# Optimization experiments

Measured on AMD Instinct MI355X. Metric: run time of the kernel, lower is better.

The kernel has to match this reference:

```python
import jax, jax.numpy as jnp
import numpy as np

H = W = 128; WS = 8; SHIFT = 4; HEADS = 4; T = 2; EPS = 1e-5
N = WS * WS  # tokens per window per frame


def _rel_pos_index(ws):
    ch, cw = np.meshgrid(np.arange(ws), np.arange(ws), indexing='ij')
    coords = np.stack([ch, cw]).reshape(2, -1)  # (2, N)
    rel = coords[:, :, None] - coords[:, None, :]  # (2, N, N)
    rel = rel.transpose(1, 2, 0)
    rel[:, :, 0] += ws - 1
    rel[:, :, 1] += ws - 1
    rel[:, :, 0] *= 2 * ws - 1
    return rel.sum(-1)  # (N, N) int


def _attn_mask(h, w, ws, shift):
    img = np.zeros((h, w))
    cnt = 0
    for hs in (slice(0, -ws), slice(-ws, -shift), slice(-shift, None)):
        for wsl in (slice(0, -ws), slice(-ws, -shift), slice(-shift, None)):
            img[hs, wsl] = cnt
            cnt += 1
    mw = img.reshape(h // ws, ws, w // ws, ws).transpose(0, 2, 1, 3).reshape(-1, ws * ws)
    diff = mw[:, None, :] - mw[:, :, None]
    return np.where(diff != 0, -100.0, 0.0).astype(np.float32)  # (nW, N, N)


REL_IDX = jnp.asarray(_rel_pos_index(WS))
ATTN_MASK = jnp.asarray(_attn_mask(H, W, WS, SHIFT))


def _ln(x, g, b):
    mu = x.mean(-1, keepdims=True)
    var = ((x - mu) ** 2).mean(-1, keepdims=True)
    return (x - mu) * jax.lax.rsqrt(var + EPS) * g + b


def setup_inputs() -> dict:
    key = jax.random.key(0)
    ks = jax.random.split(key, 8)
    B, C = 4, 128
    hid = 4 * C
    s = 0.02
    return {
        'x_v': jax.random.normal(ks[0], (B, T, H * W, C), jnp.float32),
        'qkv_w': jax.random.normal(ks[1], (3 * C, C), jnp.float32) * s,
        'qkv_b': jnp.zeros((3 * C,), jnp.float32),
        'proj_w': jax.random.normal(ks[2], (C, C), jnp.float32) * s,
        'proj_b': jnp.zeros((C,), jnp.float32),
        'rpb_table': jax.random.normal(ks[3], ((2 * WS - 1) ** 2, HEADS), jnp.float32) * s,
        'norm1_w': jnp.ones((C,), jnp.float32),
        'norm1_b': jnp.zeros((C,), jnp.float32),
        'norm2_w': jnp.ones((C,), jnp.float32),
        'norm2_b': jnp.zeros((C,), jnp.float32),
        'fc1_w': jax.random.normal(ks[4], (hid, C), jnp.float32) * s,
        'fc1_b': jnp.zeros((hid,), jnp.float32),
        'fc2_w': jax.random.normal(ks[5], (C, hid), jnp.float32) * s,
        'fc2_b': jnp.zeros((C,), jnp.float32),
    }


def reference(x_v, qkv_w, qkv_b, proj_w, proj_b, rpb_table,
              norm1_w, norm1_b, norm2_w, norm2_b,
              fc1_w, fc1_b, fc2_w, fc2_b):
    B, Tt, L, C = x_v.shape
    hd = C // HEADS
    nWh, nWw = H // WS, W // WS
    nW = nWh * nWw
    TN = T * N

    shortcut = x_v.reshape(B * T, L, C)
    x = x_v.reshape(B * T, H, W, C)
    x = jnp.roll(x, (-SHIFT, -SHIFT), axis=(1, 2))
    # window partition: (B*T, nWh, ws, nWw, ws, C) -> (B*nW, T, N, C)
    x = x.reshape(B * T, nWh, WS, nWw, WS, C).transpose(0, 1, 3, 2, 4, 5)
    x = x.reshape(B, T, nW, N, C).transpose(0, 2, 1, 3, 4).reshape(B * nW, T, N, C)

    # --- window attention over T*N tokens ---
    B_ = B * nW
    xf = x.reshape(B_, TN, C)
    qkv = xf @ qkv_w.T + qkv_b  # (B_, TN, 3C)
    qkv = qkv.reshape(B_, TN, 3, HEADS, hd).transpose(2, 0, 3, 1, 4)
    q, k, v = qkv[0], qkv[1], qkv[2]  # (B_, heads, TN, hd)
    q = q * (hd ** -0.5)
    attn = jnp.einsum('bhqd,bhkd->bhqk', q, k)  # (B_, heads, TN, TN)

    rpb = rpb_table[REL_IDX.reshape(-1)].reshape(N, N, HEADS).transpose(2, 0, 1)
    rpb = jnp.tile(rpb, (1, T, T))  # (heads, TN, TN)
    attn = attn + rpb[None]

    mask = jnp.tile(ATTN_MASK, (1, T, T))  # (nW, TN, TN)
    attn = attn.reshape(B, nW, HEADS, TN, TN) + mask[None, :, None]
    attn = jax.nn.softmax(attn.reshape(B_, HEADS, TN, TN), axis=-1)

    out = jnp.einsum('bhqk,bhkd->bhqd', attn, v)  # (B_, heads, TN, hd)
    out = out.transpose(0, 2, 1, 3).reshape(B_, T, N, C)
    out = out.reshape(B_ * T * N, C) @ proj_w.T + proj_b
    out = out.reshape(B_, T, N, C)

    # window reverse: (B*nW, T, N, C) -> (B, T, H, W, C)
    x = out.reshape(B, nWh, nWw, T, WS, WS, C).transpose(0, 3, 1, 4, 2, 5, 6)
    x = x.reshape(B * T, H, W, C)
    x = jnp.roll(x, (SHIFT, SHIFT), axis=(1, 2)).reshape(B * T, L, C)

    x = shortcut + x
    h = _ln(x, norm2_w, norm2_b)
    h = jax.nn.gelu(h @ fc1_w.T + fc1_b, approximate=False) @ fc2_w.T + fc2_b
    x = _ln(x + h, norm1_w, norm1_b)
    return x.reshape(B, T, L, C)
```

## Files before the change

### kernel.cpp

```cpp
#include <hip/hip_runtime.h>

typedef unsigned short us;
typedef short s16x8 __attribute__((ext_vector_type(8)));
typedef float f32x4 __attribute__((ext_vector_type(4)));

__device__ __forceinline__ us f2bf(float f) {
  union { float f; unsigned u; } v; v.f = f;
  unsigned u = v.u;
  u += 0x7fffu + ((u >> 16) & 1u);
  return (us)(u >> 16);
}
__device__ __forceinline__ float bf2f(us u) {
  union { unsigned u; float f; } v; v.u = ((unsigned)u) << 16; return v.f;
}
__device__ __forceinline__ s16x8 ld8(const us* p) { return *(const s16x8*)p; }

#define MFMA(a, b, c) __builtin_amdgcn_mfma_f32_16x16x32_bf16(a, b, c, 0, 0, 0)

__device__ __forceinline__ void lds_fence() {
  asm volatile("s_waitcnt lgkmcnt(0)" ::: "memory");
}

__device__ __forceinline__ float qsum(float v) {
  v += __shfl_xor(v, 1, 64); v += __shfl_xor(v, 2, 64);
  v += __shfl_xor(v, 4, 64); v += __shfl_xor(v, 8, 64);
  return v;
}

__device__ __forceinline__ float gelu_fast(float x) {
  float x2 = x * x;
  float nz = x * (-1.5957691216f - 0.0713548163f * x2);
  float e = __expf(nz);
  return x * __builtin_amdgcn_rcpf(1.f + e);
}

__global__ void prep_kernel(const float* __restrict__ qkv_w, const float* __restrict__ proj_w,
                            const float* __restrict__ fc1_w, const float* __restrict__ fc2_w,
                            const float* __restrict__ rpb_table,
                            us* __restrict__ qkvw, us* __restrict__ projw,
                            us* __restrict__ fc1w, us* __restrict__ fc2w,
                            us* __restrict__ rpbm) {
  int id = blockIdx.x * 256 + threadIdx.x;
  if (id < 49152) {
    int n = id % 384, k = id / 384;
    float v = qkv_w[n * 128 + k];
    if (n < 128) v *= 0.17677669529663687f;
    qkvw[(((k >> 3) * 384 + n) << 3) + (k & 7)] = f2bf(v);
    return;
  }
  id -= 49152;
  if (id < 16384) { int n = id % 128, k = id / 128;
    projw[(((k >> 3) * 128 + n) << 3) + (k & 7)] = f2bf(proj_w[n * 128 + k]); return; }
  id -= 16384;
  if (id < 65536) {
    int n = id % 512, k = id / 512;
    int cc = n >> 6, ni = (n >> 4) & 3, c16v = n & 15;
    int ks = k >> 5, qd = (k >> 3) & 3, j = k & 7;
    fc1w[cc * 8192 + (ks * 4 + ni) * 512 + (qd * 16 + c16v) * 8 + j] = f2bf(fc1_w[n * 128 + k]);
    return; }
  id -= 65536;
  if (id < 65536) {
    int n = id % 128, k = id / 128;
    int cc = k >> 6, ks2 = (k >> 5) & 1, qd = (k >> 3) & 3, j = k & 7;
    int ni = n >> 4, c16v = n & 15;
    fc2w[cc * 8192 + (ks2 * 8 + ni) * 512 + (qd * 16 + c16v) * 8 + j] = f2bf(fc2_w[n * 512 + k]);
    return; }
  id -= 65536;
  {
    int h = id >> 14, cls = (id >> 12) & 3, e = id & 4095;
    int n1 = e >> 6, n2 = e & 63;
    int r1 = n1 >> 3, c1 = n1 & 7, r2 = n2 >> 3, c2 = n2 & 7;
    int cH = cls >> 1, cW = cls & 1;
    int cq = (cH ? (r1 < 4 ? 1 : 2) : 0) * 3 + (cW ? (c1 < 4 ? 1 : 2) : 0);
    int ck = (cH ? (r2 < 4 ? 1 : 2) : 0) * 3 + (cW ? (c2 < 4 ? 1 : 2) : 0);
    int ridx = (r1 - r2 + 7) * 15 + (c1 - c2 + 7);
    float v = rpb_table[ridx * 4 + h] + (cq != ck ? -100.f : 0.f);
    rpbm[id] = f2bf(v);
  }
}

__global__ __launch_bounds__(512, 2) void qkv_attn_kernel(
    const float* __restrict__ x_v, const us* __restrict__ qkvw,
    const float* __restrict__ qkv_b, const us* __restrict__ rpbm,
    us* __restrict__ attn_out) {
  __shared__ __align__(16) unsigned char smem[139264];
  us* A   = (us*)smem;
  us* Qs  = (us*)smem;
  us* Ks  = (us*)(smem + 34816);
  us* Vts = (us*)(smem + 69632);

  int w = blockIdx.x;
  int b = w >> 8, wi = w & 255, wh = wi >> 4, ww = wi & 15;
  int tid = threadIdx.x;

  {
    int token = tid >> 2, q = tid & 3;
    int t = token >> 6, n = token & 63, r = n >> 3, c = n & 7;
    int hs = (wh * 8 + r + 4) & 127, wsc = (ww * 8 + c + 4) & 127;
    const float* src = x_v + (size_t)((b * 2 + t) * 16384 + hs * 128 + wsc) * 128 + q * 32;
    us* dst = A + token * 136 + q * 32;
#pragma unroll
    for (int i = 0; i < 4; ++i) {
      float4 f0 = ((const float4*)src)[2 * i];
      float4 f1 = ((const float4*)src)[2 * i + 1];
      s16x8 v;
      v[0] = (short)f2bf(f0.x); v[1] = (short)f2bf(f0.y);
      v[2] = (short)f2bf(f0.z); v[3] = (short)f2bf(f0.w);
      v[4] = (short)f2bf(f1.x); v[5] = (short)f2bf(f1.y);
      v[6] = (short)f2bf(f1.z); v[7] = (short)f2bf(f1.w);
      *(s16x8*)(dst + i * 8) = v;
    }
  }
  __syncthreads();

  int lane = tid & 63, wv = tid >> 6, quad = lane >> 4, c16 = lane & 15;
  int h = wv >> 1, p = wv & 1;
  int clsid = ((wh == 15) ? 2 : 0) + ((ww == 15) ? 1 : 0);

  int rb = p * 64;
  f32x4 acc[4][6];
#pragma unroll
  for (int mi = 0; mi < 4; ++mi)
#pragma unroll
    for (int ni = 0; ni < 6; ++ni) acc[mi][ni] = (f32x4){0.f, 0.f, 0.f, 0.f};
#pragma unroll
  for (int ks = 0; ks < 4; ++ks) {
    int k0 = ks * 32;
    s16x8 af[4];
#pragma unroll
    for (int mi = 0; mi < 4; ++mi)
      af[mi] = ld8(A + (rb + mi * 16 + c16) * 136 + k0 + quad * 8);
#pragma unroll
    for (int ni = 0; ni < 6; ++ni) {
      int gcol = (ni >> 1) * 128 + h * 32 + (ni & 1) * 16 + c16;
      s16x8 bf = ld8(qkvw + ((((k0 >> 3) + quad) * 384 + gcol) << 3));
#pragma unroll
      for (int mi = 0; mi < 4; ++mi) acc[mi][ni] = MFMA(af[mi], bf, acc[mi][ni]);
    }
  }
  __syncthreads();
#pragma unroll
  for (int ni = 0; ni < 6; ++ni) {
    int part = ni >> 1, colh = (ni & 1) * 16 + c16;
    int col = h * 32 + colh;
    float bias = qkv_b[part * 128 + col];
    if (part == 0) bias *= 0.17677669529663687f;
#pragma unroll
    for (int mi = 0; mi < 4; ++mi)
#pragma unroll
      for (int r = 0; r < 4; ++r) {
        int tok = rb + mi * 16 + quad * 4 + r;
        us v = f2bf(acc[mi][ni][r] + bias);
        if (part == 0) Qs[tok * 136 + col] = v;
        else if (part == 1) Ks[tok * 136 + col] = v;
        else Vts[col * 136 + tok] = v;
      }
  }
  __syncthreads();

  us* Pw = (us*)(smem + 104448 + wv * 4352);
  const us* rsrc = rpbm + ((h * 4 + clsid) << 12);
  int cb = h * 32;

  for (int qq = 0; qq < 4; ++qq) {
    int q0 = (p * 4 + qq) * 16;
    s16x8 aq = ld8(Qs + (q0 + c16) * 136 + cb + quad * 8);
    float rbv[8][4];
#pragma unroll
    for (int nj = 0; nj < 8; ++nj) {
      int nk = (nj * 16 + c16) & 63;
#pragma unroll
      for (int r = 0; r < 4; ++r) {
        int nq = (q0 + quad * 4 + r) & 63;
        rbv[nj][r] = bf2f(rsrc[nq * 64 + nk]);
      }
    }
    f32x4 sacc[8];
#pragma unroll
    for (int nj = 0; nj < 8; ++nj) {
      s16x8 bk = ld8(Ks + (nj * 16 + c16) * 136 + cb + quad * 8);
      f32x4 z = (f32x4){0.f, 0.f, 0.f, 0.f};
      sacc[nj] = MFMA(aq, bk, z);
    }
    float sm[4] = {0.f, 0.f, 0.f, 0.f};
#pragma unroll
    for (int nj = 0; nj < 8; ++nj)
#pragma unroll
      for (int r = 0; r < 4; ++r) {
        float pp = __expf(sacc[nj][r] + rbv[nj][r]);
        sacc[nj][r] = pp;
        sm[r] += pp;
      }
    float inv[4];
#pragma unroll
    for (int r = 0; r < 4; ++r) inv[r] = 1.f / qsum(sm[r]);
#pragma unroll
    for (int nj = 0; nj < 8; ++nj)
#pragma unroll
      for (int r = 0; r < 4; ++r)
        Pw[(quad * 4 + r) * 136 + nj * 16 + c16] = f2bf(sacc[nj][r] * inv[r]);
    lds_fence();
    f32x4 oacc[2];
    oacc[0] = (f32x4){0.f, 0.f, 0.f, 0.f};
    oacc[1] = (f32x4){0.f, 0.f, 0.f, 0.f};
#pragma unroll
    for (int ks = 0; ks < 4; ++ks) {
      int k0 = ks * 32;
      s16x8 ap = ld8(Pw + c16 * 136 + k0 + quad * 8);
#pragma unroll
      for (int nt = 0; nt < 2; ++nt) {
        s16x8 bv = ld8(Vts + (cb + nt * 16 + c16) * 136 + k0 + quad * 8);
        oacc[nt] = MFMA(ap, bv, oacc[nt]);
      }
    }
#pragma unroll
    for (int nt = 0; nt < 2; ++nt)
#pragma unroll
      for (int r = 0; r < 4; ++r) {
        int tok = q0 + quad * 4 + r;
        attn_out[((size_t)w * 128 + tok) * 128 + cb + nt * 16 + c16] =
            f2bf(oacc[nt][r]);
      }
    lds_fence();
  }
}

__global__ __launch_bounds__(256) void fused_kernel8(
    const us* __restrict__ attn_ws, const us* __restrict__ projw,
    const float* __restrict__ proj_b, const float* __restrict__ x_v,
    const us* __restrict__ fc1w, const us* __restrict__ fc2w,
    const float* __restrict__ fc1_b, const float* __restrict__ fc2_b,
    const float* __restrict__ n2w, const float* __restrict__ n2b,
    const float* __restrict__ n1w, const float* __restrict__ n1b,
    float* __restrict__ out) {
  __shared__ __align__(16) unsigned char smem[50176];
  us* A   = (us*)smem;
  us* Ws1 = (us*)(smem + 17408);
  us* Ws2 = (us*)(smem + 33792);
  int blk = blockIdx.x;
  int w = blk >> 1, hb = (blk & 1) * 64;
  int b = w >> 8, wi = w & 255, wh = wi >> 4, ww = wi & 15;
  int tid = threadIdx.x;
  int lane = tid & 63, wv = tid >> 6, quad = lane >> 4, c16 = lane & 15;
  int r0 = wv * 16;
  us* Hw = (us*)(smem + wv * 2304);

  {
    int lr = r0 + (lane >> 2), q = lane & 3;
    const us* src = attn_ws + ((size_t)w * 128 + hb + lr) * 128 + q * 32;
    us* dst = A + lr * 136 + q * 32;
#pragma unroll
    for (int i = 0; i < 4; ++i) *(s16x8*)(dst + i * 8) = ld8(src + i * 8);
  }

  size_t grow[4];
  float xv[4][8];
#pragma unroll
  for (int r = 0; r < 4; ++r) {
    int tt = hb + r0 + quad * 4 + r;
    int t = tt >> 6, n = tt & 63, rr = n >> 3, cc2 = n & 7;
    int hf = (wh * 8 + rr + 4) & 127, wf = (ww * 8 + cc2 + 4) & 127;
    grow[r] = (size_t)((b * 2 + t) * 16384 + hf * 128 + wf) * 128;
#pragma unroll
    for (int ni = 0; ni < 8; ++ni) xv[r][ni] = x_v[grow[r] + ni * 16 + c16];
  }

  s16x8 st1[4], st2[4];
  {
    const s16x8* s1 = (const s16x8*)fc1w;
    const s16x8* s2 = (const s16x8*)fc2w;
#pragma unroll
    for (int i = 0; i < 4; ++i) { st1[i] = s1[i * 256 + tid]; st2[i] = s2[i * 256 + tid]; }
  }
  lds_fence();

  f32x4 y[8];
#pragma unroll
  for (int ni = 0; ni < 8; ++ni) y[ni] = (f32x4){0.f, 0.f, 0.f, 0.f};
#pragma unroll
  for (int ks = 0; ks < 4; ++ks) {
    int k0 = ks * 32;
    s16x8 af = ld8(A + (r0 + c16) * 136 + k0 + quad * 8);
#pragma unroll
    for (int ni = 0; ni < 8; ++ni) {
      s16x8 bf = ld8(projw + ((((k0 >> 3) + quad) * 128 + ni * 16 + c16) << 3));
      y[ni] = MFMA(af, bf, y[ni]);
    }
  }

  {
    float sum[4] = {0.f, 0.f, 0.f, 0.f}, sq[4] = {0.f, 0.f, 0.f, 0.f};
#pragma unroll
    for (int ni = 0; ni < 8; ++ni) {
      float pb = proj_b[ni * 16 + c16];
#pragma unroll
      for (int r = 0; r < 4; ++r) {
        float v = y[ni][r] + pb + xv[r][ni];
        y[ni][r] = v;
        sum[r] += v; sq[r] += v * v;
      }
    }
#pragma unroll
    for (int r = 0; r < 4; ++r) {
      float s = qsum(sum[r]), q = qsum(sq[r]);
      float mean = s * 0.0078125f;
      float rstd = rsqrtf(q * 0.0078125f - mean * mean + 1e-5f);
      int m = r0 + quad * 4 + r;
#pragma unroll
      for (int ni = 0; ni < 8; ++ni) {
        int col = ni * 16 + c16;
        A[m * 136 + col] = f2bf((y[ni][r] - mean) * rstd * n2w[col] + n2b[col]);
      }
    }
  }
  lds_fence();

  s16x8 afm[4];
#pragma unroll
  for (int ks = 0; ks < 4; ++ks)
    afm[ks] = ld8(A + (r0 + c16) * 136 + ks * 32 + quad * 8);

  f32x4 o[8];
#pragma unroll
  for (int ni = 0; ni < 8; ++ni) o[ni] = (f32x4){0.f, 0.f, 0.f, 0.f};

  for (int cc = 0; cc < 8; ++cc) {
    __syncthreads();
    {
      s16x8* d1 = (s16x8*)Ws1;
      s16x8* d2 = (s16x8*)Ws2;
#pragma unroll
      for (int i = 0; i < 4; ++i) { d1[i * 256 + tid] = st1[i]; d2[i * 256 + tid] = st2[i]; }
    }
    __syncthreads();
    if (cc < 7) {
      const s16x8* s1 = (const s16x8*)fc1w + (cc + 1) * 1024;
      const s16x8* s2 = (const s16x8*)fc2w + (cc + 1) * 1024;
#pragma unroll
      for (int i = 0; i < 4; ++i) { st1[i] = s1[i * 256 + tid]; st2[i] = s2[i * 256 + tid]; }
    }
    f32x4 f[4];
#pragma unroll
    for (int ni = 0; ni < 4; ++ni) f[ni] = (f32x4){0.f, 0.f, 0.f, 0.f};
#pragma unroll
    for (int ks = 0; ks < 4; ++ks)
#pragma unroll
      for (int ni = 0; ni < 4; ++ni) {
        s16x8 bf = ld8(Ws1 + (ks * 4 + ni) * 512 + lane * 8);
        f[ni] = MFMA(afm[ks], bf, f[ni]);
      }
#pragma unroll
    for (int ni = 0; ni < 4; ++ni) {
      float bb = fc1_b[cc * 64 + ni * 16 + c16];
#pragma unroll
      for (int r = 0; r < 4; ++r) {
        float u = f[ni][r] + bb;
        Hw[(quad * 4 + r) * 72 + ni * 16 + c16] = f2bf(gelu_fast(u));
      }
    }
    lds_fence();
#pragma unroll
    for (int ks2 = 0; ks2 < 2; ++ks2) {
      s16x8 ah = ld8(Hw + c16 * 72 + ks2 * 32 + quad * 8);
#pragma unroll
      for (int ni = 0; ni < 8; ++ni) {
        s16x8 bf = ld8(Ws2 + (ks2 * 8 + ni) * 512 + lane * 8);
        o[ni] = MFMA(ah, bf, o[ni]);
      }
    }
    lds_fence();
  }

  {
    float s1v[4] = {0.f, 0.f, 0.f, 0.f}, q1[4] = {0.f, 0.f, 0.f, 0.f};
#pragma unroll
    for (int ni = 0; ni < 8; ++ni) {
      float fb = fc2_b[ni * 16 + c16];
#pragma unroll
      for (int r = 0; r < 4; ++r) {
        float v = o[ni][r] + fb + y[ni][r];
        y[ni][r] = v;
        s1v[r] += v; q1[r] += v * v;
      }
    }
#pragma unroll
    for (int r = 0; r < 4; ++r) {
      float s = qsum(s1v[r]), q = qsum(q1[r]);
      float mean = s * 0.0078125f;
      float rstd = rsqrtf(q * 0.0078125f - mean * mean + 1e-5f);
#pragma unroll
      for (int ni = 0; ni < 8; ++ni) {
        int col = ni * 16 + c16;
        out[grow[r] + col] = (y[ni][r] - mean) * rstd * n1w[col] + n1b[col];
      }
    }
  }
}

extern "C" void kernel_launch(void* const* d_in, const int* in_sizes, int n_in,
                              void* d_out, int out_size, void* d_ws, size_t ws_size,
                              hipStream_t stream) {
  const float* x_v   = (const float*)d_in[0];
  const float* qkv_w = (const float*)d_in[1];
  const float* qkv_b = (const float*)d_in[2];
  const float* proj_w = (const float*)d_in[3];
  const float* proj_b = (const float*)d_in[4];
  const float* rpb_t = (const float*)d_in[5];
  const float* n1w = (const float*)d_in[6];
  const float* n1b = (const float*)d_in[7];
  const float* n2w = (const float*)d_in[8];
  const float* n2b = (const float*)d_in[9];
  const float* fc1_w = (const float*)d_in[10];
  const float* fc1_b = (const float*)d_in[11];
  const float* fc2_w = (const float*)d_in[12];
  const float* fc2_b = (const float*)d_in[13];

  char* ws = (char*)d_ws;
  us* qkvw    = (us*)(ws + 0);
  us* projw   = (us*)(ws + 98304);
  us* fc1w    = (us*)(ws + 131072);
  us* fc2w    = (us*)(ws + 262144);
  us* rpbm    = (us*)(ws + 393216);
  us* attn_ws = (us*)(ws + 524288);

  prep_kernel<<<1024, 256, 0, stream>>>(qkv_w, proj_w, fc1_w, fc2_w, rpb_t,
                                        qkvw, projw, fc1w, fc2w, rpbm);
  qkv_attn_kernel<<<1024, 512, 0, stream>>>(x_v, qkvw, qkv_b, rpbm, attn_ws);
  fused_kernel8<<<2048, 256, 0, stream>>>(attn_ws, projw, proj_b, x_v,
                                          fc1w, fc2w, fc1_b, fc2_b,
                                          n2w, n2b, n1w, n1b, (float*)d_out);
}
```

Before: 278.3 us.

## Double-buffer MLP weight chunks in LDS and pre-swizzle bias/mask for vector loads

The MLP loop now uses 32-wide hidden chunks with two LDS buffers. The next chunk is copied from global memory straight into the alternate buffer, which removes one barrier and the register staging per iteration. The relative-position-bias/mask table is expanded in the prep kernel into a per-lane MFMA fragment layout, so each lane reads its biases with four 16-byte loads instead of 32 scalar gathers. The cost is a table four times larger, twice as many loop iterations, and global loads whose latency now sits on the barrier path.

```diff
diff --git a/kernel.cpp b/kernel.cpp
--- a/kernel.cpp
+++ b/kernel.cpp
@@ -54,28 +54,30 @@
   id -= 16384;
   if (id < 65536) {
     int n = id % 512, k = id / 512;
-    int cc = n >> 6, ni = (n >> 4) & 3, c16v = n & 15;
-    int ks = k >> 5, qd = (k >> 3) & 3, j = k & 7;
-    fc1w[cc * 8192 + (ks * 4 + ni) * 512 + (qd * 16 + c16v) * 8 + j] = f2bf(fc1_w[n * 128 + k]);
+    fc1w[((n >> 5) << 12) + (((k >> 5) * 2 + ((n >> 4) & 1)) << 9)
+         + ((((k >> 3) & 3) * 16 + (n & 15)) << 3) + (k & 7)] = f2bf(fc1_w[n * 128 + k]);
     return; }
   id -= 65536;
   if (id < 65536) {
     int n = id % 128, k = id / 128;
-    int cc = k >> 6, ks2 = (k >> 5) & 1, qd = (k >> 3) & 3, j = k & 7;
-    int ni = n >> 4, c16v = n & 15;
-    fc2w[cc * 8192 + (ks2 * 8 + ni) * 512 + (qd * 16 + c16v) * 8 + j] = f2bf(fc2_w[n * 512 + k]);
+    fc2w[((k >> 5) << 12) + ((n >> 4) << 9)
+         + ((((k >> 3) & 3) * 16 + (n & 15)) << 3) + (k & 7)] = f2bf(fc2_w[n * 512 + k]);
     return; }
   id -= 65536;
   {
-    int h = id >> 14, cls = (id >> 12) & 3, e = id & 4095;
-    int n1 = e >> 6, n2 = e & 63;
-    int r1 = n1 >> 3, c1 = n1 & 7, r2 = n2 >> 3, c2 = n2 & 7;
+    int h = id >> 15, cls = (id >> 13) & 3, qcase = (id >> 11) & 3;
+    int lane = (id >> 5) & 63, v = id & 31;
+    int nj = v >> 2, rr = v & 3;
+    int quad = lane >> 4, c16v = lane & 15;
+    int nq = (qcase * 16 + quad * 4 + rr) & 63;
+    int nk = (nj * 16 + c16v) & 63;
+    int r1 = nq >> 3, c1 = nq & 7, r2 = nk >> 3, c2 = nk & 7;
     int cH = cls >> 1, cW = cls & 1;
     int cq = (cH ? (r1 < 4 ? 1 : 2) : 0) * 3 + (cW ? (c1 < 4 ? 1 : 2) : 0);
     int ck = (cH ? (r2 < 4 ? 1 : 2) : 0) * 3 + (cW ? (c2 < 4 ? 1 : 2) : 0);
     int ridx = (r1 - r2 + 7) * 15 + (c1 - c2 + 7);
-    float v = rpb_table[ridx * 4 + h] + (cq != ck ? -100.f : 0.f);
-    rpbm[id] = f2bf(v);
+    float val = rpb_table[ridx * 4 + h] + (cq != ck ? -100.f : 0.f);
+    rpbm[id] = f2bf(val);
   }
 }
 
@@ -159,22 +161,16 @@
   __syncthreads();
 
   us* Pw = (us*)(smem + 104448 + wv * 4352);
-  const us* rsrc = rpbm + ((h * 4 + clsid) << 12);
+  const us* rsrc = rpbm + (((h * 4 + clsid) * 4) << 11) + lane * 32;
   int cb = h * 32;
 
   for (int qq = 0; qq < 4; ++qq) {
     int q0 = (p * 4 + qq) * 16;
     s16x8 aq = ld8(Qs + (q0 + c16) * 136 + cb + quad * 8);
-    float rbv[8][4];
-#pragma unroll
-    for (int nj = 0; nj < 8; ++nj) {
-      int nk = (nj * 16 + c16) & 63;
-#pragma unroll
-      for (int r = 0; r < 4; ++r) {
-        int nq = (q0 + quad * 4 + r) & 63;
-        rbv[nj][r] = bf2f(rsrc[nq * 64 + nk]);
-      }
-    }
+    const us* rp = rsrc + (((q0 >> 4) & 3) << 11);
+    s16x8 rbv8[4];
+#pragma unroll
+    for (int i = 0; i < 4; ++i) rbv8[i] = ld8(rp + i * 8);
     f32x4 sacc[8];
 #pragma unroll
     for (int nj = 0; nj < 8; ++nj) {
@@ -187,7 +183,7 @@
     for (int nj = 0; nj < 8; ++nj)
 #pragma unroll
       for (int r = 0; r < 4; ++r) {
-        float pp = __expf(sacc[nj][r] + rbv[nj][r]);
+        float pp = __expf(sacc[nj][r] + bf2f((us)rbv8[nj >> 1][((nj & 1) << 2) + r]));
         sacc[nj][r] = pp;
         sm[r] += pp;
       }
@@ -225,7 +221,7 @@
   }
 }
 
-__global__ __launch_bounds__(256) void fused_kernel8(
+__global__ __launch_bounds__(256) void fused_kernel9(
     const us* __restrict__ attn_ws, const us* __restrict__ projw,
     const float* __restrict__ proj_b, const float* __restrict__ x_v,
     const us* __restrict__ fc1w, const us* __restrict__ fc2w,
@@ -234,16 +230,16 @@
     const float* __restrict__ n1w, const float* __restrict__ n1b,
     float* __restrict__ out) {
   __shared__ __align__(16) unsigned char smem[50176];
-  us* A   = (us*)smem;
-  us* Ws1 = (us*)(smem + 17408);
-  us* Ws2 = (us*)(smem + 33792);
+  us* A  = (us*)smem;
+  us* W1 = (us*)(smem + 17408);
+  us* W2 = (us*)(smem + 33792);
   int blk = blockIdx.x;
   int w = blk >> 1, hb = (blk & 1) * 64;
   int b = w >> 8, wi = w & 255, wh = wi >> 4, ww = wi & 15;
   int tid = threadIdx.x;
   int lane = tid & 63, wv = tid >> 6, quad = lane >> 4, c16 = lane & 15;
   int r0 = wv * 16;
-  us* Hw = (us*)(smem + wv * 2304);
+  us* Hw = (us*)(smem + wv * 1280);
 
   {
     int lr = r0 + (lane >> 2), q = lane & 3;
@@ -265,12 +261,14 @@
     for (int ni = 0; ni < 8; ++ni) xv[r][ni] = x_v[grow[r] + ni * 16 + c16];
   }
 
-  s16x8 st1[4], st2[4];
   {
     const s16x8* s1 = (const s16x8*)fc1w;
     const s16x8* s2 = (const s16x8*)fc2w;
-#pragma unroll
-    for (int i = 0; i < 4; ++i) { st1[i] = s1[i * 256 + tid]; st2[i] = s2[i * 256 + tid]; }
+    s16x8* d1 = (s16x8*)W1;
+    s16x8* d2 = (s16x8*)W2;
+#pragma unroll
+    for (int i = 0; i < 2; ++i) { d1[i * 256 + tid] = s1[i * 256 + tid];
+                                  d2[i * 256 + tid] = s2[i * 256 + tid]; }
   }
   lds_fence();
 
@@ -324,49 +322,43 @@
 #pragma unroll
   for (int ni = 0; ni < 8; ++ni) o[ni] = (f32x4){0.f, 0.f, 0.f, 0.f};
 
-  for (int cc = 0; cc < 8; ++cc) {
+  for (int cc = 0; cc < 16; ++cc) {
+    int cur = cc & 1;
     __syncthreads();
-    {
-      s16x8* d1 = (s16x8*)Ws1;
-      s16x8* d2 = (s16x8*)Ws2;
-#pragma unroll
-      for (int i = 0; i < 4; ++i) { d1[i * 256 + tid] = st1[i]; d2[i * 256 + tid] = st2[i]; }
-    }
-    __syncthreads();
-    if (cc < 7) {
-      const s16x8* s1 = (const s16x8*)fc1w + (cc + 1) * 1024;
-      const s16x8* s2 = (const s16x8*)fc2w + (cc + 1) * 1024;
-#pragma unroll
-      for (int i = 0; i < 4; ++i) { st1[i] = s1[i * 256 + tid]; st2[i] = s2[i * 256 + tid]; }
-    }
-    f32x4 f[4];
-#pragma unroll
-    for (int ni = 0; ni < 4; ++ni) f[ni] = (f32x4){0.f, 0.f, 0.f, 0.f};
+    if (cc < 15) {
+      const s16x8* s1 = (const s16x8*)(fc1w + ((cc + 1) << 12));
+      const s16x8* s2 = (const s16x8*)(fc2w + ((cc + 1) << 12));
+      s16x8* d1 = (s16x8*)(W1 + ((cur ^ 1) << 12));
+      s16x8* d2 = (s16x8*)(W2 + ((cur ^ 1) << 12));
+#pragma unroll
+      for (int i = 0; i < 2; ++i) { d1[i * 256 + tid] = s1[i * 256 + tid];
+                                    d2[i * 256 + tid] = s2[i * 256 + tid]; }
+    }
+    const us* w1c = W1 + (cur << 12);
+    const us* w2c = W2 + (cur << 12);
+    f32x4 f[2];
+    f[0] = (f32x4){0.f, 0.f, 0.f, 0.f};
+    f[1] = (f32x4){0.f, 0.f, 0.f, 0.f};
 #pragma unroll
     for (int ks = 0; ks < 4; ++ks)
 #pragma unroll
-      for (int ni = 0; ni < 4; ++ni) {
-        s16x8 bf = ld8(Ws1 + (ks * 4 + ni) * 512 + lane * 8);
+      for (int ni = 0; ni < 2; ++ni) {
+        s16x8 bf = ld8(w1c + ((ks * 2 + ni) << 9) + lane * 8);
         f[ni] = MFMA(afm[ks], bf, f[ni]);
       }
 #pragma unroll
-    for (int ni = 0; ni < 4; ++ni) {
-      float bb = fc1_b[cc * 64 + ni * 16 + c16];
-#pragma unroll
-      for (int r = 0; r < 4; ++r) {
-        float u = f[ni][r] + bb;
-        Hw[(quad * 4 + r) * 72 + ni * 16 + c16] = f2bf(gelu_fast(u));
-      }
+    for (int ni = 0; ni < 2; ++ni) {
+      float bb = fc1_b[cc * 32 + ni * 16 + c16];
+#pragma unroll
+      for (int r = 0; r < 4; ++r)
+        Hw[(quad * 4 + r) * 40 + ni * 16 + c16] = f2bf(gelu_fast(f[ni][r] + bb));
     }
     lds_fence();
-#pragma unroll
-    for (int ks2 = 0; ks2 < 2; ++ks2) {
-      s16x8 ah = ld8(Hw + c16 * 72 + ks2 * 32 + quad * 8);
-#pragma unroll
-      for (int ni = 0; ni < 8; ++ni) {
-        s16x8 bf = ld8(Ws2 + (ks2 * 8 + ni) * 512 + lane * 8);
-        o[ni] = MFMA(ah, bf, o[ni]);
-      }
+    s16x8 ah = ld8(Hw + c16 * 40 + quad * 8);
+#pragma unroll
+    for (int ni = 0; ni < 8; ++ni) {
+      s16x8 bf = ld8(w2c + (ni << 9) + lane * 8);
+      o[ni] = MFMA(ah, bf, o[ni]);
     }
     lds_fence();
   }
@@ -421,12 +413,12 @@
   us* fc1w    = (us*)(ws + 131072);
   us* fc2w    = (us*)(ws + 262144);
   us* rpbm    = (us*)(ws + 393216);
-  us* attn_ws = (us*)(ws + 524288);
-
-  prep_kernel<<<1024, 256, 0, stream>>>(qkv_w, proj_w, fc1_w, fc2_w, rpb_t,
+  us* attn_ws = (us*)(ws + 655360);
+
+  prep_kernel<<<1280, 256, 0, stream>>>(qkv_w, proj_w, fc1_w, fc2_w, rpb_t,
                                         qkvw, projw, fc1w, fc2w, rpbm);
   qkv_attn_kernel<<<1024, 512, 0, stream>>>(x_v, qkvw, qkv_b, rpbm, attn_ws);
-  fused_kernel8<<<2048, 256, 0, stream>>>(attn_ws, projw, proj_b, x_v,
+  fused_kernel9<<<2048, 256, 0, stream>>>(attn_ws, projw, proj_b, x_v,
                                           fc1w, fc2w, fc1_b, fc2_b,
                                           n2w, n2b, n1w, n1b, (float*)d_out);
 }
```

Result: slower. 294.1 us (+5.7%).

## Fuse attention and MLP kernels into one window-level mega kernel

Applied to the files above, without the earlier changes.

Merges the QKV/attention kernel and the proj+MLP kernel into a single kernel per window, keeping the attention output in LDS instead of writing it to a global workspace and reading it back. The rel-pos-bias/mask table is re-laid-out in prep so each lane reads its bias values as contiguous 8-element vectors, and Q fragments are hoisted into registers. The MLP weight chunks are now copied straight from global into LDS each iteration instead of being staged through registers. This removes a launch and a round trip through global memory. In exchange, blocks now hold 512 threads with 136KB of LDS, and the two-blocks-per-CU launch bound is dropped, which may lower occupancy and register headroom.

```diff
diff --git a/kernel.cpp b/kernel.cpp
--- a/kernel.cpp
+++ b/kernel.cpp
@@ -67,27 +67,37 @@
     return; }
   id -= 65536;
   {
-    int h = id >> 14, cls = (id >> 12) & 3, e = id & 4095;
-    int n1 = e >> 6, n2 = e & 63;
-    int r1 = n1 >> 3, c1 = n1 & 7, r2 = n2 >> 3, c2 = n2 & 7;
+    int h = id >> 15, cls = (id >> 13) & 3, qcase = (id >> 11) & 3;
+    int lane = (id >> 5) & 63, v = id & 31;
+    int nj = v >> 2, rr = v & 3;
+    int quad = lane >> 4, c16v = lane & 15;
+    int nq = (qcase * 16 + quad * 4 + rr) & 63;
+    int nk = (nj * 16 + c16v) & 63;
+    int r1 = nq >> 3, c1 = nq & 7, r2 = nk >> 3, c2 = nk & 7;
     int cH = cls >> 1, cW = cls & 1;
     int cq = (cH ? (r1 < 4 ? 1 : 2) : 0) * 3 + (cW ? (c1 < 4 ? 1 : 2) : 0);
     int ck = (cH ? (r2 < 4 ? 1 : 2) : 0) * 3 + (cW ? (c2 < 4 ? 1 : 2) : 0);
     int ridx = (r1 - r2 + 7) * 15 + (c1 - c2 + 7);
-    float v = rpb_table[ridx * 4 + h] + (cq != ck ? -100.f : 0.f);
-    rpbm[id] = f2bf(v);
-  }
-}
-
-__global__ __launch_bounds__(512, 2) void qkv_attn_kernel(
+    float val = rpb_table[ridx * 4 + h] + (cq != ck ? -100.f : 0.f);
+    rpbm[id] = f2bf(val);
+  }
+}
+
+__global__ __launch_bounds__(512) void mega_kernel(
     const float* __restrict__ x_v, const us* __restrict__ qkvw,
     const float* __restrict__ qkv_b, const us* __restrict__ rpbm,
-    us* __restrict__ attn_out) {
+    const us* __restrict__ projw, const float* __restrict__ proj_b,
+    const us* __restrict__ fc1w, const us* __restrict__ fc2w,
+    const float* __restrict__ fc1_b, const float* __restrict__ fc2_b,
+    const float* __restrict__ n2w, const float* __restrict__ n2b,
+    const float* __restrict__ n1w, const float* __restrict__ n1b,
+    float* __restrict__ out) {
   __shared__ __align__(16) unsigned char smem[139264];
   us* A   = (us*)smem;
-  us* Qs  = (us*)smem;
   us* Ks  = (us*)(smem + 34816);
   us* Vts = (us*)(smem + 69632);
+  us* W1  = (us*)(smem + 34816);
+  us* W2  = (us*)(smem + 34816 + 16384);
 
   int w = blockIdx.x;
   int b = w >> 8, wi = w & 255, wh = wi >> 4, ww = wi & 15;
@@ -116,78 +126,79 @@
   int lane = tid & 63, wv = tid >> 6, quad = lane >> 4, c16 = lane & 15;
   int h = wv >> 1, p = wv & 1;
   int clsid = ((wh == 15) ? 2 : 0) + ((ww == 15) ? 1 : 0);
-
-  int rb = p * 64;
-  f32x4 acc[4][6];
-#pragma unroll
-  for (int mi = 0; mi < 4; ++mi)
-#pragma unroll
-    for (int ni = 0; ni < 6; ++ni) acc[mi][ni] = (f32x4){0.f, 0.f, 0.f, 0.f};
-#pragma unroll
-  for (int ks = 0; ks < 4; ++ks) {
-    int k0 = ks * 32;
-    s16x8 af[4];
+  int cb = h * 32;
+
+  {
+    int rb = p * 64;
+    f32x4 acc[4][6];
 #pragma unroll
     for (int mi = 0; mi < 4; ++mi)
-      af[mi] = ld8(A + (rb + mi * 16 + c16) * 136 + k0 + quad * 8);
+#pragma unroll
+      for (int ni = 0; ni < 6; ++ni) acc[mi][ni] = (f32x4){0.f, 0.f, 0.f, 0.f};
+#pragma unroll
+    for (int ks = 0; ks < 4; ++ks) {
+      int k0 = ks * 32;
+      s16x8 af[4];
+#pragma unroll
+      for (int mi = 0; mi < 4; ++mi)
+        af[mi] = ld8(A + (rb + mi * 16 + c16) * 136 + k0 + quad * 8);
+#pragma unroll
+      for (int ni = 0; ni < 6; ++ni) {
+        int gcol = (ni >> 1) * 128 + cb + (ni & 1) * 16 + c16;
+        s16x8 bf = ld8(qkvw + ((((k0 >> 3) + quad) * 384 + gcol) << 3));
+#pragma unroll
+        for (int mi = 0; mi < 4; ++mi) acc[mi][ni] = MFMA(af[mi], bf, acc[mi][ni]);
+      }
+    }
+    __syncthreads();
 #pragma unroll
     for (int ni = 0; ni < 6; ++ni) {
-      int gcol = (ni >> 1) * 128 + h * 32 + (ni & 1) * 16 + c16;
-      s16x8 bf = ld8(qkvw + ((((k0 >> 3) + quad) * 384 + gcol) << 3));
-#pragma unroll
-      for (int mi = 0; mi < 4; ++mi) acc[mi][ni] = MFMA(af[mi], bf, acc[mi][ni]);
+      int part = ni >> 1, colh = (ni & 1) * 16 + c16;
+      int col = cb + colh;
+      float bias = qkv_b[part * 128 + col];
+      if (part == 0) bias *= 0.17677669529663687f;
+#pragma unroll
+      for (int mi = 0; mi < 4; ++mi)
+#pragma unroll
+        for (int r = 0; r < 4; ++r) {
+          int tok = rb + mi * 16 + quad * 4 + r;
+          us v = f2bf(acc[mi][ni][r] + bias);
+          if (part == 0) A[tok * 136 + col] = v;
+          else if (part == 1) Ks[tok * 136 + col] = v;
+          else Vts[col * 136 + tok] = v;
+        }
     }
   }
   __syncthreads();
-#pragma unroll
-  for (int ni = 0; ni < 6; ++ni) {
-    int part = ni >> 1, colh = (ni & 1) * 16 + c16;
-    int col = h * 32 + colh;
-    float bias = qkv_b[part * 128 + col];
-    if (part == 0) bias *= 0.17677669529663687f;
-#pragma unroll
-    for (int mi = 0; mi < 4; ++mi)
-#pragma unroll
-      for (int r = 0; r < 4; ++r) {
-        int tok = rb + mi * 16 + quad * 4 + r;
-        us v = f2bf(acc[mi][ni][r] + bias);
-        if (part == 0) Qs[tok * 136 + col] = v;
-        else if (part == 1) Ks[tok * 136 + col] = v;
-        else Vts[col * 136 + tok] = v;
-      }
-  }
+
+  s16x8 aq[4];
+#pragma unroll
+  for (int qq = 0; qq < 4; ++qq)
+    aq[qq] = ld8(A + ((p * 4 + qq) * 16 + c16) * 136 + cb + quad * 8);
   __syncthreads();
 
   us* Pw = (us*)(smem + 104448 + wv * 4352);
-  const us* rsrc = rpbm + ((h * 4 + clsid) << 12);
-  int cb = h * 32;
+  const us* rsrc = rpbm + (((h * 4 + clsid) * 4) << 11) + lane * 32;
 
   for (int qq = 0; qq < 4; ++qq) {
     int q0 = (p * 4 + qq) * 16;
-    s16x8 aq = ld8(Qs + (q0 + c16) * 136 + cb + quad * 8);
-    float rbv[8][4];
-#pragma unroll
-    for (int nj = 0; nj < 8; ++nj) {
-      int nk = (nj * 16 + c16) & 63;
-#pragma unroll
-      for (int r = 0; r < 4; ++r) {
-        int nq = (q0 + quad * 4 + r) & 63;
-        rbv[nj][r] = bf2f(rsrc[nq * 64 + nk]);
-      }
-    }
+    const us* rp = rsrc + (((q0 >> 4) & 3) << 11);
+    s16x8 rbv8[4];
+#pragma unroll
+    for (int i = 0; i < 4; ++i) rbv8[i] = ld8(rp + i * 8);
     f32x4 sacc[8];
 #pragma unroll
     for (int nj = 0; nj < 8; ++nj) {
       s16x8 bk = ld8(Ks + (nj * 16 + c16) * 136 + cb + quad * 8);
       f32x4 z = (f32x4){0.f, 0.f, 0.f, 0.f};
-      sacc[nj] = MFMA(aq, bk, z);
+      sacc[nj] = MFMA(aq[qq], bk, z);
     }
     float sm[4] = {0.f, 0.f, 0.f, 0.f};
 #pragma unroll
     for (int nj = 0; nj < 8; ++nj)
 #pragma unroll
       for (int r = 0; r < 4; ++r) {
-        float pp = __expf(sacc[nj][r] + rbv[nj][r]);
+        float pp = __expf(sacc[nj][r] + bf2f((us)rbv8[nj >> 1][((nj & 1) << 2) + r]));
         sacc[nj][r] = pp;
         sm[r] += pp;
       }
@@ -218,46 +229,20 @@
 #pragma unroll
       for (int r = 0; r < 4; ++r) {
         int tok = q0 + quad * 4 + r;
-        attn_out[((size_t)w * 128 + tok) * 128 + cb + nt * 16 + c16] =
-            f2bf(oacc[nt][r]);
+        A[tok * 136 + cb + nt * 16 + c16] = f2bf(oacc[nt][r]);
       }
     lds_fence();
   }
-}
-
-__global__ __launch_bounds__(256) void fused_kernel8(
-    const us* __restrict__ attn_ws, const us* __restrict__ projw,
-    const float* __restrict__ proj_b, const float* __restrict__ x_v,
-    const us* __restrict__ fc1w, const us* __restrict__ fc2w,
-    const float* __restrict__ fc1_b, const float* __restrict__ fc2_b,
-    const float* __restrict__ n2w, const float* __restrict__ n2b,
-    const float* __restrict__ n1w, const float* __restrict__ n1b,
-    float* __restrict__ out) {
-  __shared__ __align__(16) unsigned char smem[50176];
-  us* A   = (us*)smem;
-  us* Ws1 = (us*)(smem + 17408);
-  us* Ws2 = (us*)(smem + 33792);
-  int blk = blockIdx.x;
-  int w = blk >> 1, hb = (blk & 1) * 64;
-  int b = w >> 8, wi = w & 255, wh = wi >> 4, ww = wi & 15;
-  int tid = threadIdx.x;
-  int lane = tid & 63, wv = tid >> 6, quad = lane >> 4, c16 = lane & 15;
+  __syncthreads();
+
   int r0 = wv * 16;
-  us* Hw = (us*)(smem + wv * 2304);
-
-  {
-    int lr = r0 + (lane >> 2), q = lane & 3;
-    const us* src = attn_ws + ((size_t)w * 128 + hb + lr) * 128 + q * 32;
-    us* dst = A + lr * 136 + q * 32;
-#pragma unroll
-    for (int i = 0; i < 4; ++i) *(s16x8*)(dst + i * 8) = ld8(src + i * 8);
-  }
+  us* Hw = (us*)(smem + 69632 + wv * 2304);
 
   size_t grow[4];
   float xv[4][8];
 #pragma unroll
   for (int r = 0; r < 4; ++r) {
-    int tt = hb + r0 + quad * 4 + r;
+    int tt = r0 + quad * 4 + r;
     int t = tt >> 6, n = tt & 63, rr = n >> 3, cc2 = n & 7;
     int hf = (wh * 8 + rr + 4) & 127, wf = (ww * 8 + cc2 + 4) & 127;
     grow[r] = (size_t)((b * 2 + t) * 16384 + hf * 128 + wf) * 128;
@@ -265,14 +250,15 @@
     for (int ni = 0; ni < 8; ++ni) xv[r][ni] = x_v[grow[r] + ni * 16 + c16];
   }
 
-  s16x8 st1[4], st2[4];
   {
     const s16x8* s1 = (const s16x8*)fc1w;
     const s16x8* s2 = (const s16x8*)fc2w;
-#pragma unroll
-    for (int i = 0; i < 4; ++i) { st1[i] = s1[i * 256 + tid]; st2[i] = s2[i * 256 + tid]; }
-  }
-  lds_fence();
+    s16x8* d1 = (s16x8*)W1;
+    s16x8* d2 = (s16x8*)W2;
+#pragma unroll
+    for (int i = 0; i < 2; ++i) { d1[i * 512 + tid] = s1[i * 512 + tid];
+                                  d2[i * 512 + tid] = s2[i * 512 + tid]; }
+  }
 
   f32x4 y[8];
 #pragma unroll
@@ -326,19 +312,6 @@
 
   for (int cc = 0; cc < 8; ++cc) {
     __syncthreads();
-    {
-      s16x8* d1 = (s16x8*)Ws1;
-      s16x8* d2 = (s16x8*)Ws2;
-#pragma unroll
-      for (int i = 0; i < 4; ++i) { d1[i * 256 + tid] = st1[i]; d2[i * 256 + tid] = st2[i]; }
-    }
-    __syncthreads();
-    if (cc < 7) {
-      const s16x8* s1 = (const s16x8*)fc1w + (cc + 1) * 1024;
-      const s16x8* s2 = (const s16x8*)fc2w + (cc + 1) * 1024;
-#pragma unroll
-      for (int i = 0; i < 4; ++i) { st1[i] = s1[i * 256 + tid]; st2[i] = s2[i * 256 + tid]; }
-    }
     f32x4 f[4];
 #pragma unroll
     for (int ni = 0; ni < 4; ++ni) f[ni] = (f32x4){0.f, 0.f, 0.f, 0.f};
@@ -346,7 +319,7 @@
     for (int ks = 0; ks < 4; ++ks)
 #pragma unroll
       for (int ni = 0; ni < 4; ++ni) {
-        s16x8 bf = ld8(Ws1 + (ks * 4 + ni) * 512 + lane * 8);
+        s16x8 bf = ld8(W1 + (ks * 4 + ni) * 512 + lane * 8);
         f[ni] = MFMA(afm[ks], bf, f[ni]);
       }
 #pragma unroll
@@ -364,11 +337,22 @@
       s16x8 ah = ld8(Hw + c16 * 72 + ks2 * 32 + quad * 8);
 #pragma unroll
       for (int ni = 0; ni < 8; ++ni) {
-        s16x8 bf = ld8(Ws2 + (ks2 * 8 + ni) * 512 + lane * 8);
+        s16x8 bf = ld8(W2 + (ks2 * 8 + ni) * 512 + lane * 8);
         o[ni] = MFMA(ah, bf, o[ni]);
       }
     }
-    lds_fence();
+    if (cc < 7) {
+      __syncthreads();
+      const s16x8* s1 = (const s16x8*)fc1w + (cc + 1) * 1024;
+      const s16x8* s2 = (const s16x8*)fc2w + (cc + 1) * 1024;
+      s16x8* d1 = (s16x8*)W1;
+      s16x8* d2 = (s16x8*)W2;
+#pragma unroll
+      for (int i = 0; i < 2; ++i) { d1[i * 512 + tid] = s1[i * 512 + tid];
+                                    d2[i * 512 + tid] = s2[i * 512 + tid]; }
+    } else {
+      lds_fence();
+    }
   }
 
   {
@@ -421,12 +405,10 @@
   us* fc1w    = (us*)(ws + 131072);
   us* fc2w    = (us*)(ws + 262144);
   us* rpbm    = (us*)(ws + 393216);
-  us* attn_ws = (us*)(ws + 524288);
-
-  prep_kernel<<<1024, 256, 0, stream>>>(qkv_w, proj_w, fc1_w, fc2_w, rpb_t,
+
+  prep_kernel<<<1280, 256, 0, stream>>>(qkv_w, proj_w, fc1_w, fc2_w, rpb_t,
                                         qkvw, projw, fc1w, fc2w, rpbm);
-  qkv_attn_kernel<<<1024, 512, 0, stream>>>(x_v, qkvw, qkv_b, rpbm, attn_ws);
-  fused_kernel8<<<2048, 256, 0, stream>>>(attn_ws, projw, proj_b, x_v,
-                                          fc1w, fc2w, fc1_b, fc2_b,
-                                          n2w, n2b, n1w, n1b, (float*)d_out);
-}
+  mega_kernel<<<1024, 512, 0, stream>>>(x_v, qkvw, qkv_b, rpbm,
+                                        projw, proj_b, fc1w, fc2w, fc1_b, fc2_b,
+                                        n2w, n2b, n1w, n1b, (float*)d_out);
+}
```

New measurement: 309.6 us. 1.11x slower.
